# Kernel optimization log

Measured on AMD Instinct MI355X. Metric: run time of the kernel, lower is better.

## Reference

```python
import jax, jax.numpy as jnp
import numpy as np

HEAD = 16
NEG = -1.0e9


def setup_inputs() -> dict:
    key = jax.random.key(0)
    ks = jax.random.split(key, 8)
    B, S, D = 2, 2048, 1024
    scale = 1.0 / np.sqrt(D)
    inp = {
        "query": jax.random.normal(ks[0], (B, S, D), jnp.float32),
        "key": jax.random.normal(ks[1], (B, S, D), jnp.float32),
        "value": jax.random.normal(ks[2], (B, S, D), jnp.float32),
        "mask": jnp.ones((B, S, S), jnp.int32),
        "w_q": jax.random.normal(ks[3], (D, D), jnp.float32) * scale,
        "b_q": jnp.zeros((D,), jnp.float32),
        "w_k": jax.random.normal(ks[4], (D, D), jnp.float32) * scale,
        "b_k": jnp.zeros((D,), jnp.float32),
        "w_v": jax.random.normal(ks[5], (D, D), jnp.float32) * scale,
        "b_v": jnp.zeros((D,), jnp.float32),
        "w_o": jax.random.normal(ks[6], (D, D), jnp.float32) * scale,
        "b_o": jnp.zeros((D,), jnp.float32),
    }
    return inp


def _split_heads(x, B, S, H, dk):
    # [B,S,D] -> [B,H,S,dk]
    return x.reshape(B, S, H, dk).transpose(0, 2, 1, 3)


def reference(query, key, value, mask, w_q, b_q, w_k, b_k, w_v, b_v, w_o, b_o):
    B, S, D = query.shape
    H = HEAD
    dk = D // H
    q = _split_heads(query @ w_q.T + b_q, B, S, H, dk)
    k = _split_heads(key @ w_k.T + b_k, B, S, H, dk)
    v = _split_heads(value @ w_v.T + b_v, B, S, H, dk)
    # scores: [B,H,S,S]
    scores = jnp.einsum('bhqd,bhkd->bhqk', q, k) / jnp.sqrt(jnp.float32(dk))
    scores = jnp.where(mask[:, None, :, :] == 0, NEG, scores)
    p = jax.nn.softmax(scores, axis=-1)  # dropout is identity in eval
    x = jnp.einsum('bhqk,bhkd->bhqd', p, v)  # [B,H,S,dk]
    x = x.transpose(0, 2, 1, 3).reshape(B, S, D)
    return x @ w_o.T + b_o
```

## Files before the change

kernel.cpp:

```cpp
#include <hip/hip_runtime.h>

typedef float f32x4 __attribute__((ext_vector_type(4)));
typedef short bf16x8 __attribute__((ext_vector_type(8)));
typedef unsigned short u16x4 __attribute__((ext_vector_type(4)));

#define BB 2
#define SS 2048
#define DM 1024
#define NH 16
#define DKH 64
#define MROWS 4096

__device__ __forceinline__ unsigned short f2bf(float x) {
  union { float f; unsigned int u; } v; v.f = x;
  unsigned int r = v.u + 0x7fffu + ((v.u >> 16) & 1u);
  return (unsigned short)(r >> 16);
}

__device__ __forceinline__ void gll16(const void* g, void* l) {
  __builtin_amdgcn_global_load_lds(
      (const __attribute__((address_space(1))) void*)g,
      (__attribute__((address_space(3))) void*)l, 16, 0, 0);
}

template <int C>
__device__ __forceinline__ float dppf(float x) {
  return __builtin_bit_cast(float,
      __builtin_amdgcn_mov_dpp(__builtin_bit_cast(int, x), C, 0xf, 0xf, true));
}
__device__ __forceinline__ float rowmax16(float v) {
  v = fmaxf(v, dppf<0xB1>(v));
  v = fmaxf(v, dppf<0x4E>(v));
  v = fmaxf(v, dppf<0x141>(v));
  v = fmaxf(v, dppf<0x140>(v));
  return v;
}
__device__ __forceinline__ float rowsum16(float v) {
  v += dppf<0xB1>(v);
  v += dppf<0x4E>(v);
  v += dppf<0x141>(v);
  v += dppf<0x140>(v);
  return v;
}

struct CvtArgs {
  const float* src[7];
  unsigned short* dst[7];
  int n4[7];
};

__global__ __launch_bounds__(256) void cvt7_kernel(CvtArgs a) {
  const int z = blockIdx.y;
  const int i = blockIdx.x * 256 + threadIdx.x;
  if (i >= a.n4[z]) return;
  f32x4 v = ((const f32x4*)a.src[z])[i];
  u16x4 o;
  o[0] = f2bf(v[0]); o[1] = f2bf(v[1]); o[2] = f2bf(v[2]); o[3] = f2bf(v[3]);
  ((u16x4*)a.dst[z])[i] = o;
}

__global__ __launch_bounds__(256) void init_out_kernel(const float* __restrict__ b_o,
                                                       float* __restrict__ out) {
  const int i = blockIdx.x * 256 + threadIdx.x;
  ((f32x4*)out)[i] = ((const f32x4*)b_o)[i & 255];
}

__global__ __launch_bounds__(256) void mask_flags_kernel(const int* __restrict__ mask,
                                                         int* __restrict__ flags) {
  const int bid = blockIdx.x;
  const int b = bid >> 8, qt = (bid >> 4) & 15, kt = bid & 15;
  __shared__ int sf;
  if (threadIdx.x == 0) sf = 0;
  __syncthreads();
  int any0 = 0;
  const size_t base = ((size_t)b * SS + qt * 128) * SS + kt * 128;
  for (int p = 0; p < 64; ++p) {
    int i = p * 256 + threadIdx.x;
    int r = i >> 7, col = i & 127;
    any0 |= (mask[base + (size_t)r * SS + col] == 0);
  }
  if (any0) sf = 1;
  __syncthreads();
  if (threadIdx.x == 0) flags[bid] = sf;
}

struct ProjArgs {
  const unsigned short* A[3];
  const unsigned short* W[3];
  const float* bias[3];
  void* out[3];
  float alpha[3];
  int mode[3];
  int kstart[3];
  int kcount[3];
};

__global__ __launch_bounds__(256, 3) void proj_gemm(ProjArgs args) {
  __shared__ unsigned short As[128][32];
  __shared__ unsigned short Bs[128][32];
  const int z = blockIdx.z;
  const unsigned short* __restrict__ A = args.A[z];
  const unsigned short* __restrict__ W = args.W[z];
  const float* __restrict__ bias = args.bias[z];
  const float alpha = args.alpha[z];
  const int mode = args.mode[z];
  const int kbeg = args.kstart[z], kend = args.kstart[z] + args.kcount[z];

  const int tid = threadIdx.x;
  const int w = tid >> 6, lane = tid & 63;
  const int quad = lane >> 4, c = lane & 15;
  const int m0 = blockIdx.x * 128, n0 = blockIdx.y * 128;
  const int wm = (w >> 1) * 64, wn = (w & 1) * 64;
  const int sr = lane >> 2, scc = lane & 3;
  const int lx = scc ^ ((sr >> 1) & 3);
  const int sk = (quad ^ ((c >> 1) & 3)) * 8;

  f32x4 acc[4][4];
#pragma unroll
  for (int i = 0; i < 4; ++i)
#pragma unroll
    for (int j = 0; j < 4; ++j) { f32x4 zz = {0.f, 0.f, 0.f, 0.f}; acc[i][j] = zz; }

  for (int kt = kbeg; kt < kend; ++kt) {
    const int k0 = kt * 32;
    __syncthreads();
#pragma unroll
    for (int t = 0; t < 2; ++t) {
      const int tt = w + t * 4;
      const int r = tt * 16 + sr;
      gll16(A + (size_t)(m0 + r) * DM + k0 + lx * 8, &As[r][scc * 8]);
      gll16(W + (size_t)(n0 + r) * DM + k0 + lx * 8, &Bs[r][scc * 8]);
    }
    __syncthreads();
    bf16x8 af[4], bfr[4];
#pragma unroll
    for (int i = 0; i < 4; ++i) af[i] = *(const bf16x8*)&As[wm + i * 16 + c][sk];
#pragma unroll
    for (int j = 0; j < 4; ++j) bfr[j] = *(const bf16x8*)&Bs[wn + j * 16 + c][sk];
#pragma unroll
    for (int i = 0; i < 4; ++i)
#pragma unroll
      for (int j = 0; j < 4; ++j)
        acc[i][j] = __builtin_amdgcn_mfma_f32_16x16x32_bf16(af[i], bfr[j], acc[i][j], 0, 0, 0);
  }

#pragma unroll
  for (int i = 0; i < 4; ++i)
#pragma unroll
    for (int j = 0; j < 4; ++j)
#pragma unroll
      for (int r = 0; r < 4; ++r) {
        const int m = m0 + wm + i * 16 + quad * 4 + r;
        const int n = n0 + wn + j * 16 + c;
        if (mode == 3) {
          atomicAdd(&((float*)args.out[z])[(size_t)m * DM + n], acc[i][j][r]);
          continue;
        }
        const float val = (acc[i][j][r] + bias[n]) * alpha;
        if (mode == 2) {
          ((float*)args.out[z])[(size_t)m * DM + n] = val;
        } else {
          const int bb = m >> 11, s = m & 2047, hh = n >> 6, d = n & 63;
          size_t idx;
          if (mode == 0) {
            idx = (((size_t)(bb * NH + hh)) * SS + s) * DKH + d;
          } else {
            const int sl = s & 127, blk = s >> 7;
            const int jj = sl >> 4, rem = sl & 15, kc = rem >> 2, qd = rem & 3;
            const int pos = kc * 32 + qd * 8 + jj;
            idx = (((size_t)(bb * NH + hh)) * DKH + d) * SS + blk * 128 + pos;
          }
          ((unsigned short*)args.out[z])[idx] = f2bf(val);
        }
      }
}

__global__ __launch_bounds__(256, 2) void attn_kernel(
    const unsigned short* __restrict__ qp, const unsigned short* __restrict__ kp,
    const unsigned short* __restrict__ vtp, const int* __restrict__ mask,
    const int* __restrict__ flags, unsigned short* __restrict__ xb) {
  __shared__ __align__(16) char smem[65536];
  unsigned short (*Ks)[128][32] = (unsigned short (*)[128][32])smem;
  unsigned short (*Vt)[64][32]  = (unsigned short (*)[64][32])(smem + 16384);
  unsigned short (*Qs)[128][32] = (unsigned short (*)[128][32])(smem + 32768);
  unsigned short (*Ps)[128]     = (unsigned short (*)[128])(smem + 32768);

  const int tid = threadIdx.x;
  const int w = tid >> 6, lane = tid & 63;
  const int quad = lane >> 4, c = lane & 15;
  const int qt = blockIdx.x, bh = blockIdx.y;
  const int b = bh >> 4, h = bh & 15;
  const int q0 = qt * 128;
  const int sr = lane >> 2, scc = lane & 3;
  const int lx = scc ^ ((sr >> 1) & 3);
  const int sk = (quad ^ ((c >> 1) & 3)) * 8;

#pragma unroll
  for (int t = 0; t < 4; ++t) {
    const int tt = w * 4 + t;
    const int kk = tt >> 3;
    const int r = (tt & 7) * 16 + sr;
    gll16(qp + ((size_t)bh * SS + q0 + r) * DKH + kk * 32 + lx * 8, &Qs[kk][r][scc * 8]);
  }
  __syncthreads();
  bf16x8 aq[2][2];
#pragma unroll
  for (int rt = 0; rt < 2; ++rt)
#pragma unroll
    for (int kk = 0; kk < 2; ++kk)
      aq[rt][kk] = *(const bf16x8*)&Qs[kk][w * 32 + rt * 16 + c][sk];

  f32x4 acco[2][4];
#pragma unroll
  for (int rt = 0; rt < 2; ++rt)
#pragma unroll
    for (int j = 0; j < 4; ++j) { f32x4 zz = {0.f, 0.f, 0.f, 0.f}; acco[rt][j] = zz; }
  float m_run[2][4], l_run[2][4];
#pragma unroll
  for (int rt = 0; rt < 2; ++rt)
#pragma unroll
    for (int r = 0; r < 4; ++r) { m_run[rt][r] = -3.0e38f; l_run[rt][r] = 0.f; }

  for (int kt = 0; kt < 16; ++kt) {
    const int k0 = kt * 128;
    __syncthreads();
#pragma unroll
    for (int i = 0; i < 4; ++i) {
      const int tt = w * 4 + i;
      {
        const int kk = tt >> 3, r = (tt & 7) * 16 + sr;
        gll16(kp + ((size_t)bh * SS + k0 + r) * DKH + kk * 32 + lx * 8, &Ks[kk][r][scc * 8]);
      }
      {
        const int kc = tt >> 2, d = (tt & 3) * 16 + sr;
        gll16(vtp + ((size_t)bh * DKH + d) * SS + k0 + kc * 32 + lx * 8, &Vt[kc][d][scc * 8]);
      }
    }
    __syncthreads();

    f32x4 accs[2][8];
#pragma unroll
    for (int rt = 0; rt < 2; ++rt)
#pragma unroll
      for (int j = 0; j < 8; ++j) { f32x4 zz = {0.f, 0.f, 0.f, 0.f}; accs[rt][j] = zz; }
#pragma unroll
    for (int j = 0; j < 8; ++j) {
      const int rowk = j * 16 + c;
      const bf16x8 bk0 = *(const bf16x8*)&Ks[0][rowk][sk];
      const bf16x8 bk1 = *(const bf16x8*)&Ks[1][rowk][sk];
#pragma unroll
      for (int rt = 0; rt < 2; ++rt) {
        accs[rt][j] = __builtin_amdgcn_mfma_f32_16x16x32_bf16(aq[rt][0], bk0, accs[rt][j], 0, 0, 0);
        accs[rt][j] = __builtin_amdgcn_mfma_f32_16x16x32_bf16(aq[rt][1], bk1, accs[rt][j], 0, 0, 0);
      }
    }

    if (flags[((size_t)b * 16 + qt) * 16 + kt]) {
#pragma unroll
      for (int rt = 0; rt < 2; ++rt)
#pragma unroll
        for (int j = 0; j < 8; ++j)
#pragma unroll
          for (int r = 0; r < 4; ++r) {
            const int qq = q0 + w * 32 + rt * 16 + quad * 4 + r;
            const int kk2 = k0 + j * 16 + c;
            if (mask[((size_t)b * SS + qq) * SS + kk2] == 0) accs[rt][j][r] = -1.0e30f;
          }
    }

    float al[2][4];
#pragma unroll
    for (int rt = 0; rt < 2; ++rt)
#pragma unroll
      for (int r = 0; r < 4; ++r) {
        float v = accs[rt][0][r];
#pragma unroll
        for (int j = 1; j < 8; ++j) v = fmaxf(v, accs[rt][j][r]);
        v = rowmax16(v);
        const float mn = fmaxf(m_run[rt][r], v);
        al[rt][r] = __builtin_amdgcn_exp2f(m_run[rt][r] - mn);
        m_run[rt][r] = mn;
        float s = 0.f;
        union { bf16x8 v8; unsigned short u[8]; } pk;
#pragma unroll
        for (int j = 0; j < 8; ++j) {
          const float p = __builtin_amdgcn_exp2f(accs[rt][j][r] - mn);
          union { float f; unsigned int u; } pv; pv.f = p;
          pk.u[j] = (unsigned short)(pv.u >> 16);
          union { unsigned int u; float f; } pr; pr.u = pv.u & 0xffff0000u;
          s += pr.f;
        }
        const int prow = w * 32 + rt * 16 + quad * 4 + r;
        *(bf16x8*)&Ps[prow][(c ^ ((prow >> 1) & 7)) * 8] = pk.v8;
        s = rowsum16(s);
        l_run[rt][r] = l_run[rt][r] * al[rt][r] + s;
      }
#pragma unroll
    for (int rt = 0; rt < 2; ++rt)
#pragma unroll
      for (int j = 0; j < 4; ++j)
#pragma unroll
        for (int r = 0; r < 4; ++r) acco[rt][j][r] *= al[rt][r];

#pragma unroll
    for (int kc = 0; kc < 4; ++kc) {
      const int pc = ((kc * 4 + quad) ^ ((c >> 1) & 7)) * 8;
      const bf16x8 ap0 = *(const bf16x8*)&Ps[w * 32 + c][pc];
      const bf16x8 ap1 = *(const bf16x8*)&Ps[w * 32 + 16 + c][pc];
#pragma unroll
      for (int j = 0; j < 4; ++j) {
        const bf16x8 bv = *(const bf16x8*)&Vt[kc][j * 16 + c][sk];
        acco[0][j] = __builtin_amdgcn_mfma_f32_16x16x32_bf16(ap0, bv, acco[0][j], 0, 0, 0);
        acco[1][j] = __builtin_amdgcn_mfma_f32_16x16x32_bf16(ap1, bv, acco[1][j], 0, 0, 0);
      }
    }
  }

#pragma unroll
  for (int rt = 0; rt < 2; ++rt)
#pragma unroll
    for (int r = 0; r < 4; ++r) {
      const float inv = 1.0f / l_run[rt][r];
      const int q = q0 + w * 32 + rt * 16 + quad * 4 + r;
#pragma unroll
      for (int j = 0; j < 4; ++j) {
        xb[((size_t)b * SS + q) * DM + h * DKH + j * 16 + c] = f2bf(acco[rt][j][r] * inv);
      }
    }
}

extern "C" void kernel_launch(void* const* d_in, const int* in_sizes, int n_in,
                              void* d_out, int out_size, void* d_ws, size_t ws_size,
                              hipStream_t stream) {
  (void)in_sizes; (void)n_in; (void)out_size; (void)ws_size;
  const float* query = (const float*)d_in[0];
  const float* key_  = (const float*)d_in[1];
  const float* value = (const float*)d_in[2];
  const int*   mask  = (const int*)d_in[3];
  const float* w_q = (const float*)d_in[4];
  const float* b_q = (const float*)d_in[5];
  const float* w_k = (const float*)d_in[6];
  const float* b_k = (const float*)d_in[7];
  const float* w_v = (const float*)d_in[8];
  const float* b_v = (const float*)d_in[9];
  const float* w_o = (const float*)d_in[10];
  const float* b_o = (const float*)d_in[11];

  char* ws = (char*)d_ws;
  const size_t SZ_IN = (size_t)MROWS * DM * 2;
  const size_t SZ_W  = (size_t)DM * DM * 2;
  unsigned short* qin = (unsigned short*)(ws);
  unsigned short* kin = (unsigned short*)(ws + SZ_IN);
  unsigned short* vin = (unsigned short*)(ws + 2 * SZ_IN);
  unsigned short* wqb = (unsigned short*)(ws + 3 * SZ_IN);
  unsigned short* wkb = (unsigned short*)(ws + 3 * SZ_IN + SZ_W);
  unsigned short* wvb = (unsigned short*)(ws + 3 * SZ_IN + 2 * SZ_W);
  unsigned short* wob = (unsigned short*)(ws + 3 * SZ_IN + 3 * SZ_W);
  unsigned short* qp  = (unsigned short*)(ws + 3 * SZ_IN + 4 * SZ_W);
  unsigned short* kp  = (unsigned short*)(ws + 4 * SZ_IN + 4 * SZ_W);
  unsigned short* vtp = (unsigned short*)(ws + 5 * SZ_IN + 4 * SZ_W);
  unsigned short* xb  = (unsigned short*)(ws + 6 * SZ_IN + 4 * SZ_W);
  int* flags          = (int*)(ws + 7 * SZ_IN + 4 * SZ_W);

  CvtArgs ca;
  ca.src[0] = query; ca.src[1] = key_; ca.src[2] = value;
  ca.src[3] = w_q; ca.src[4] = w_k; ca.src[5] = w_v; ca.src[6] = w_o;
  ca.dst[0] = qin; ca.dst[1] = kin; ca.dst[2] = vin;
  ca.dst[3] = wqb; ca.dst[4] = wkb; ca.dst[5] = wvb; ca.dst[6] = wob;
  ca.n4[0] = ca.n4[1] = ca.n4[2] = MROWS * DM / 4;
  ca.n4[3] = ca.n4[4] = ca.n4[5] = ca.n4[6] = DM * DM / 4;
  cvt7_kernel<<<dim3(4096, 7), 256, 0, stream>>>(ca);

  init_out_kernel<<<dim3(4096), 256, 0, stream>>>(b_o, (float*)d_out);

  mask_flags_kernel<<<dim3(512), 256, 0, stream>>>(mask, flags);

  ProjArgs pa;
  pa.A[0] = qin; pa.A[1] = kin; pa.A[2] = vin;
  pa.W[0] = wqb; pa.W[1] = wkb; pa.W[2] = wvb;
  pa.bias[0] = b_q; pa.bias[1] = b_k; pa.bias[2] = b_v;
  pa.out[0] = qp; pa.out[1] = kp; pa.out[2] = vtp;
  pa.alpha[0] = 0.18033688011112042f; pa.alpha[1] = 1.f; pa.alpha[2] = 1.f;
  pa.mode[0] = 0; pa.mode[1] = 0; pa.mode[2] = 1;
  pa.kstart[0] = pa.kstart[1] = pa.kstart[2] = 0;
  pa.kcount[0] = pa.kcount[1] = pa.kcount[2] = 32;
  proj_gemm<<<dim3(32, 8, 3), 256, 0, stream>>>(pa);

  attn_kernel<<<dim3(16, 32), 256, 0, stream>>>(qp, kp, vtp, mask, flags, xb);

  ProjArgs po;
  po.A[0] = po.A[1] = po.A[2] = xb;
  po.W[0] = po.W[1] = po.W[2] = wob;
  po.bias[0] = po.bias[1] = po.bias[2] = b_o;
  po.out[0] = po.out[1] = po.out[2] = d_out;
  po.alpha[0] = po.alpha[1] = po.alpha[2] = 1.f;
  po.mode[0] = po.mode[1] = po.mode[2] = 3;
  po.kstart[0] = 0; po.kstart[1] = 16; po.kstart[2] = 0;
  po.kcount[0] = po.kcount[1] = 16; po.kcount[2] = 32;
  proj_gemm<<<dim3(32, 8, 2), 256, 0, stream>>>(po);
}
```

Baseline: 309.8 us.

## Drop split-K atomics in output projection and coalesce V-transpose stores via LDS

Result: faster. 279.2 us (-9.9%).

```diff
diff --git a/kernel.cpp b/kernel.cpp
--- a/kernel.cpp
+++ b/kernel.cpp
@@ -57,12 +57,6 @@
   u16x4 o;
   o[0] = f2bf(v[0]); o[1] = f2bf(v[1]); o[2] = f2bf(v[2]); o[3] = f2bf(v[3]);
   ((u16x4*)a.dst[z])[i] = o;
-}
-
-__global__ __launch_bounds__(256) void init_out_kernel(const float* __restrict__ b_o,
-                                                       float* __restrict__ out) {
-  const int i = blockIdx.x * 256 + threadIdx.x;
-  ((f32x4*)out)[i] = ((const f32x4*)b_o)[i & 255];
 }
 
 __global__ __launch_bounds__(256) void mask_flags_kernel(const int* __restrict__ mask,
@@ -91,20 +85,20 @@
   void* out[3];
   float alpha[3];
   int mode[3];
-  int kstart[3];
-  int kcount[3];
 };
 
 __global__ __launch_bounds__(256, 3) void proj_gemm(ProjArgs args) {
-  __shared__ unsigned short As[128][32];
-  __shared__ unsigned short Bs[128][32];
+  __shared__ __align__(16) char pbuf[17408];
+  unsigned short (*As)[32] = (unsigned short (*)[32])pbuf;
+  unsigned short (*Bs)[32] = (unsigned short (*)[32])(pbuf + 8192);
+  unsigned short (*T)[136] = (unsigned short (*)[136])pbuf;
+
   const int z = blockIdx.z;
   const unsigned short* __restrict__ A = args.A[z];
   const unsigned short* __restrict__ W = args.W[z];
   const float* __restrict__ bias = args.bias[z];
   const float alpha = args.alpha[z];
   const int mode = args.mode[z];
-  const int kbeg = args.kstart[z], kend = args.kstart[z] + args.kcount[z];
 
   const int tid = threadIdx.x;
   const int w = tid >> 6, lane = tid & 63;
@@ -121,7 +115,7 @@
 #pragma unroll
     for (int j = 0; j < 4; ++j) { f32x4 zz = {0.f, 0.f, 0.f, 0.f}; acc[i][j] = zz; }
 
-  for (int kt = kbeg; kt < kend; ++kt) {
+  for (int kt = 0; kt < 32; ++kt) {
     const int k0 = kt * 32;
     __syncthreads();
 #pragma unroll
@@ -144,6 +138,38 @@
         acc[i][j] = __builtin_amdgcn_mfma_f32_16x16x32_bf16(af[i], bfr[j], acc[i][j], 0, 0, 0);
   }
 
+  if (mode == 1) {
+    unsigned short* outp = (unsigned short*)args.out[z];
+    const int bb = m0 >> 11, sblk = (m0 >> 7) & 15;
+#pragma unroll
+    for (int h = 0; h < 2; ++h) {
+      __syncthreads();
+      if ((w & 1) == h) {
+#pragma unroll
+        for (int j = 0; j < 4; ++j) {
+          const int row = j * 16 + c;
+          const float bn = bias[n0 + h * 64 + row];
+#pragma unroll
+          for (int r = 0; r < 4; ++r) {
+            u16x4 pkt;
+#pragma unroll
+            for (int i = 0; i < 4; ++i) pkt[i] = f2bf((acc[i][j][r] + bn) * alpha);
+            *(u16x4*)&T[row][quad * 32 + r * 8 + (w >> 1) * 4] = pkt;
+          }
+        }
+      }
+      __syncthreads();
+      const int row = tid >> 2, seg = tid & 3;
+      const int n = n0 + h * 64 + row;
+      const int hh = n >> 6, d = n & 63;
+      const size_t gb = (((size_t)(bb * NH + hh)) * DKH + d) * SS + sblk * 128;
+#pragma unroll
+      for (int q = 0; q < 4; ++q)
+        *(bf16x8*)&outp[gb + (seg + 4 * q) * 8] = *(const bf16x8*)&T[row][(seg + 4 * q) * 8];
+    }
+    return;
+  }
+
 #pragma unroll
   for (int i = 0; i < 4; ++i)
 #pragma unroll
@@ -152,24 +178,12 @@
       for (int r = 0; r < 4; ++r) {
         const int m = m0 + wm + i * 16 + quad * 4 + r;
         const int n = n0 + wn + j * 16 + c;
-        if (mode == 3) {
-          atomicAdd(&((float*)args.out[z])[(size_t)m * DM + n], acc[i][j][r]);
-          continue;
-        }
         const float val = (acc[i][j][r] + bias[n]) * alpha;
         if (mode == 2) {
           ((float*)args.out[z])[(size_t)m * DM + n] = val;
         } else {
           const int bb = m >> 11, s = m & 2047, hh = n >> 6, d = n & 63;
-          size_t idx;
-          if (mode == 0) {
-            idx = (((size_t)(bb * NH + hh)) * SS + s) * DKH + d;
-          } else {
-            const int sl = s & 127, blk = s >> 7;
-            const int jj = sl >> 4, rem = sl & 15, kc = rem >> 2, qd = rem & 3;
-            const int pos = kc * 32 + qd * 8 + jj;
-            idx = (((size_t)(bb * NH + hh)) * DKH + d) * SS + blk * 128 + pos;
-          }
+          const size_t idx = (((size_t)(bb * NH + hh)) * SS + s) * DKH + d;
           ((unsigned short*)args.out[z])[idx] = f2bf(val);
         }
       }
@@ -371,8 +385,6 @@
   ca.n4[3] = ca.n4[4] = ca.n4[5] = ca.n4[6] = DM * DM / 4;
   cvt7_kernel<<<dim3(4096, 7), 256, 0, stream>>>(ca);
 
-  init_out_kernel<<<dim3(4096), 256, 0, stream>>>(b_o, (float*)d_out);
-
   mask_flags_kernel<<<dim3(512), 256, 0, stream>>>(mask, flags);
 
   ProjArgs pa;
@@ -382,8 +394,6 @@
   pa.out[0] = qp; pa.out[1] = kp; pa.out[2] = vtp;
   pa.alpha[0] = 0.18033688011112042f; pa.alpha[1] = 1.f; pa.alpha[2] = 1.f;
   pa.mode[0] = 0; pa.mode[1] = 0; pa.mode[2] = 1;
-  pa.kstart[0] = pa.kstart[1] = pa.kstart[2] = 0;
-  pa.kcount[0] = pa.kcount[1] = pa.kcount[2] = 32;
   proj_gemm<<<dim3(32, 8, 3), 256, 0, stream>>>(pa);
 
   attn_kernel<<<dim3(16, 32), 256, 0, stream>>>(qp, kp, vtp, mask, flags, xb);
@@ -394,8 +404,6 @@
   po.bias[0] = po.bias[1] = po.bias[2] = b_o;
   po.out[0] = po.out[1] = po.out[2] = d_out;
   po.alpha[0] = po.alpha[1] = po.alpha[2] = 1.f;
-  po.mode[0] = po.mode[1] = po.mode[2] = 3;
-  po.kstart[0] = 0; po.kstart[1] = 16; po.kstart[2] = 0;
-  po.kcount[0] = po.kcount[1] = 16; po.kcount[2] = 32;
-  proj_gemm<<<dim3(32, 8, 2), 256, 0, stream>>>(po);
-}
+  po.mode[0] = po.mode[1] = po.mode[2] = 2;
+  proj_gemm<<<dim3(32, 8, 1), 256, 0, stream>>>(po);
+}
```
